# Kernel optimization log

Hardware: AMD Instinct MI355X
Metric: run time of the kernel (lower is better)

## Reference

```python
import jax, jax.numpy as jnp
import numpy as np

H = 16
D_MODEL = 1024
BLOCK_SIZE = 64
B, S = 2, 2048
NEG = -65504.0  # value used by the torch module for masking


def setup_inputs() -> dict:
    key = jax.random.key(0)
    ks = jax.random.split(key, 12)
    scale = 1.0 / np.sqrt(D_MODEL)
    inp = {
        "query": jax.random.normal(ks[0], (B, S, D_MODEL), jnp.float32),
        "key": jax.random.normal(ks[1], (B, S, D_MODEL), jnp.float32),
        "value": jax.random.normal(ks[2], (B, S, D_MODEL), jnp.float32),
        "Wq": jax.random.normal(ks[3], (D_MODEL, D_MODEL), jnp.float32) * scale,
        "bq": jnp.zeros((D_MODEL,), jnp.float32),
        "Wk": jax.random.normal(ks[4], (D_MODEL, D_MODEL), jnp.float32) * scale,
        "bk": jnp.zeros((D_MODEL,), jnp.float32),
        "Wv": jax.random.normal(ks[5], (D_MODEL, D_MODEL), jnp.float32) * scale,
        "bv": jnp.zeros((D_MODEL,), jnp.float32),
        "Wo": jax.random.normal(ks[6], (D_MODEL, D_MODEL), jnp.float32) * scale,
        "bo": jnp.zeros((D_MODEL,), jnp.float32),
    }
    return inp


def reference(query, key, value, Wq, bq, Wk, bk, Wv, bv, Wo, bo):
    b, s, d = query.shape
    dk = d // H

    def proj(x, W, bias):
        # [b,s,d] -> [b,h,s,dk]
        return (x @ W + bias).reshape(b, s, H, dk).transpose(0, 2, 1, 3)

    q = proj(query, Wq, bq)
    k = proj(key, Wk, bk)
    v = proj(value, Wv, bv)

    # dense QK^T / sqrt(d_k), exactly as the torch module (then block mask added)
    scores = jnp.einsum("bhqd,bhkd->bhqk", q, k) / jnp.sqrt(jnp.float32(dk))

    bid = jnp.arange(s) // BLOCK_SIZE
    attn_mask = jnp.where(bid[:, None] == bid[None, :], 0.0, NEG).astype(scores.dtype)
    scores = scores + attn_mask  # broadcast over [b,h]

    attn = jax.nn.softmax(scores, axis=-1)
    x = jnp.einsum("bhqk,bhkd->bhqd", attn, v)
    x = x.transpose(0, 2, 1, 3).reshape(b, s, d)
    return x @ Wo + bo
```

## Files before the change

### kernel.cpp

```cpp
#include <hip/hip_runtime.h>
#include <hip/hip_bf16.h>

typedef __attribute__((ext_vector_type(4))) float f32x4;
typedef __attribute__((ext_vector_type(8))) short s16x8;

#define MFMA16(a, b, c) __builtin_amdgcn_mfma_f32_16x16x32_bf16(a, b, c, 0, 0, 0)

__device__ __forceinline__ void gld_lds16(const void* g, void* l) {
  __builtin_amdgcn_global_load_lds(
      (const __attribute__((address_space(1))) unsigned int*)g,
      (__attribute__((address_space(3))) unsigned int*)l, 16, 0, 0);
}

__device__ __forceinline__ unsigned short f2bf(float f) {
  union { __hip_bfloat16 b; unsigned short u; } cv;
  cv.b = __float2bfloat16(f);
  return cv.u;
}
__device__ __forceinline__ float bf2f(unsigned short u) {
  union { unsigned short u; __hip_bfloat16 b; } cv;
  cv.u = u;
  return __bfloat162float(cv.b);
}

__global__ void transw(const float* W0, unsigned short* H0,
                       const float* W1, unsigned short* H1,
                       const float* W2, unsigned short* H2,
                       const float* W3, unsigned short* H3) {
  __shared__ float tile[64 * 65];
  const float* W; unsigned short* H;
  switch (blockIdx.y) {
    case 0: W = W0; H = H0; break;
    case 1: W = W1; H = H1; break;
    case 2: W = W2; H = H2; break;
    default: W = W3; H = H3; break;
  }
  const int t = threadIdx.x;
  const int tk0 = (blockIdx.x & 15) * 64;
  const int tn0 = (blockIdx.x >> 4) * 64;
  for (int i = 0; i < 16; ++i) {
    int idx = i * 256 + t;
    int r = idx >> 6, c = idx & 63;
    tile[r * 65 + c] = W[(size_t)(tk0 + r) * 1024 + tn0 + c];
  }
  __syncthreads();
  for (int i = 0; i < 16; ++i) {
    int idx = i * 256 + t;
    int r = idx >> 6, c = idx & 63;
    H[(size_t)(tn0 + r) * 1024 + tk0 + c] = f2bf(tile[c * 65 + r]);
  }
}

__global__ void convert_x3(const float* A0, unsigned short* H0,
                           const float* A1, unsigned short* H1,
                           const float* A2, unsigned short* H2) {
  const float* src; unsigned short* h;
  switch (blockIdx.y) {
    case 0: src = A0; h = H0; break;
    case 1: src = A1; h = H1; break;
    default: src = A2; h = H2; break;
  }
  int i = blockIdx.x * 256 + threadIdx.x;
  float4 v = ((const float4*)src)[i];
  ((ushort4*)h)[i] = make_ushort4(f2bf(v.x), f2bf(v.y), f2bf(v.z), f2bf(v.w));
}

struct QkvArgs {
  const unsigned short* A[3];
  const unsigned short* B[3];
  const float* bias[3];
  unsigned short* out[3];
};

__global__ __launch_bounds__(512, 2)
void gemm_qkv(QkvArgs args) {
  const int K = 1024;
  __shared__ __align__(16) unsigned short lds[4][2][8192];
  const int tid = threadIdx.x;
  const int lane = tid & 63, w = tid >> 6;

  const int nwg = 192;
  const int orig = blockIdx.x;
  const int swz = (orig & 7) * (nwg >> 3) + (orig >> 3);
  const int g = swz >> 6;
  const int tl = swz & 63;
  const int m0 = (tl >> 2) * 256, n0 = (tl & 3) * 256;

  const unsigned short* A = args.A[g];
  const unsigned short* B = args.B[g];
  const float* bias = args.bias[g];
  unsigned short* out = args.out[g];

  const int wm = (w >> 2) * 128, wn = (w & 3) * 64;
  const int fr = lane & 15, gh = lane >> 4;

  size_t aoff[2], boff[2]; int dst[2];
  #pragma unroll
  for (int i = 0; i < 2; ++i) {
    const int G = i * 512 + tid;
    const int rp = G >> 3, spr = G & 7;
    const int s = spr ^ (rp & 7);
    const int srow = 2 * rp + (s >> 2), ko = (s & 3) * 8;
    aoff[i] = (size_t)(m0 + srow) * K + ko;
    boff[i] = (size_t)(n0 + srow) * K + ko;
    dst[i] = G * 8;
  }

  auto stageA = [&](int buf, int kt) {
    gld_lds16(A + aoff[0] + kt, &lds[buf][0][dst[0]]);
    gld_lds16(A + aoff[1] + kt, &lds[buf][0][dst[1]]);
  };
  auto stageB = [&](int buf, int kt) {
    gld_lds16(B + boff[0] + kt, &lds[buf][1][dst[0]]);
    gld_lds16(B + boff[1] + kt, &lds[buf][1][dst[1]]);
  };

  f32x4 acc[8][4] = {};
  const int laneoff = (fr >> 1) * 64 + ((((fr & 1) << 2) | gh) ^ (fr >> 1)) * 8;

  stageA(0, 0);  stageB(0, 0);
  stageA(1, 32); stageB(1, 32);
  stageA(2, 64); stageB(2, 64);
  asm volatile("s_waitcnt vmcnt(8)" ::: "memory");
  __builtin_amdgcn_s_barrier();
  __builtin_amdgcn_sched_barrier(0);

  #pragma unroll 1
  for (int t = 0; t < 32; ++t) {
    const int buf = t & 3;
    const unsigned short* La = &lds[buf][0][wm * 32 + laneoff];
    const unsigned short* Lb = &lds[buf][1][wn * 32 + laneoff];
    s16x8 a[8], b[4];

    #pragma unroll
    for (int nt = 0; nt < 4; ++nt) b[nt] = *(const s16x8*)&Lb[nt * 512];
    #pragma unroll
    for (int mt = 0; mt < 4; ++mt) a[mt] = *(const s16x8*)&La[mt * 512];
    if (t <= 28) stageA((t + 3) & 3, (t + 3) * 32);
    __builtin_amdgcn_s_barrier();
    asm volatile("s_waitcnt lgkmcnt(0)" ::: "memory");
    __builtin_amdgcn_sched_barrier(0);
    __builtin_amdgcn_s_setprio(1);
    #pragma unroll
    for (int mt = 0; mt < 4; ++mt)
      #pragma unroll
      for (int nt = 0; nt < 4; ++nt)
        acc[mt][nt] = MFMA16(a[mt], b[nt], acc[mt][nt]);
    __builtin_amdgcn_s_setprio(0);
    __builtin_amdgcn_s_barrier();
    __builtin_amdgcn_sched_barrier(0);

    #pragma unroll
    for (int mt = 4; mt < 8; ++mt) a[mt] = *(const s16x8*)&La[mt * 512];
    if (t <= 28) stageB((t + 3) & 3, (t + 3) * 32);
    __builtin_amdgcn_s_barrier();
    asm volatile("s_waitcnt lgkmcnt(0)" ::: "memory");
    __builtin_amdgcn_sched_barrier(0);
    __builtin_amdgcn_s_setprio(1);
    #pragma unroll
    for (int mt = 4; mt < 8; ++mt)
      #pragma unroll
      for (int nt = 0; nt < 4; ++nt)
        acc[mt][nt] = MFMA16(a[mt], b[nt], acc[mt][nt]);
    __builtin_amdgcn_s_setprio(0);
    if (t < 29)       { asm volatile("s_waitcnt vmcnt(8)" ::: "memory"); }
    else if (t == 29) { asm volatile("s_waitcnt vmcnt(4)" ::: "memory"); }
    else if (t == 30) { asm volatile("s_waitcnt vmcnt(0)" ::: "memory"); }
    __builtin_amdgcn_s_barrier();
    __builtin_amdgcn_sched_barrier(0);
  }

  float bv[4];
  #pragma unroll
  for (int nt = 0; nt < 4; ++nt) bv[nt] = bias[n0 + wn + nt * 16 + fr];
  if (g == 2) {
    #pragma unroll
    for (int mt = 0; mt < 8; ++mt) {
      const int gm = m0 + wm + mt * 16 + (gh << 2);
      const int b2 = gm >> 11, s = gm & 2047;
      #pragma unroll
      for (int nt = 0; nt < 4; ++nt) {
        const int gn = n0 + wn + nt * 16 + fr;
        const int h = gn >> 6, d = gn & 63;
        f32x4 r = acc[mt][nt];
        ushort4 w4 = make_ushort4(f2bf(r[0] + bv[nt]), f2bf(r[1] + bv[nt]),
                                  f2bf(r[2] + bv[nt]), f2bf(r[3] + bv[nt]));
        *(ushort4*)&out[((size_t)((b2 * 16 + h) * 64 + d)) * 2048 + s] = w4;
      }
    }
  } else {
    #pragma unroll
    for (int mt = 0; mt < 8; ++mt) {
      const int gm = m0 + wm + mt * 16 + (gh << 2);
      #pragma unroll
      for (int nt = 0; nt < 4; ++nt) {
        const int gn = n0 + wn + nt * 16 + fr;
        f32x4 r = acc[mt][nt];
        #pragma unroll
        for (int j = 0; j < 4; ++j) {
          const int row = gm + j;
          size_t off = (((size_t)((row >> 11) * 16 + (gn >> 6))) * 2048 + (row & 2047)) * 64 + (gn & 63);
          out[off] = f2bf(r[j] + bv[nt]);
        }
      }
    }
  }
}

__global__ __launch_bounds__(256, 3)
void gemm_oproj(const unsigned short* __restrict__ A, const unsigned short* __restrict__ B,
                const float* __restrict__ bias, float* __restrict__ out) {
  const int K = 1024, N = 1024;
  __shared__ __align__(16) unsigned short lds[3][2][4096];
  const int tid = threadIdx.x;
  const int lane = tid & 63, wid = tid >> 6;

  const int nwg = 256;
  const int orig = blockIdx.x;
  const int swz = (orig & 7) * (nwg >> 3) + (orig >> 3);
  const int m0 = (swz >> 3) * 128, n0 = (swz & 7) * 128;

  const int wm = (wid >> 1) * 64, wn = (wid & 1) * 64;
  const int fr = lane & 15, gh = lane >> 4;

  size_t aoff[2], boff[2]; int dst[2];
  #pragma unroll
  for (int i = 0; i < 2; ++i) {
    const int G = i * 256 + tid;
    const int rp = G >> 3, spr = G & 7;
    const int s = spr ^ (rp & 7);
    const int srow = 2 * rp + (s >> 2), ko = (s & 3) * 8;
    aoff[i] = (size_t)(m0 + srow) * K + ko;
    boff[i] = (size_t)(n0 + srow) * K + ko;
    dst[i] = G * 8;
  }

  auto stage = [&](int buf, int kt) {
    #pragma unroll
    for (int i = 0; i < 2; ++i) {
      gld_lds16(A + aoff[i] + kt, &lds[buf][0][dst[i]]);
      gld_lds16(B + boff[i] + kt, &lds[buf][1][dst[i]]);
    }
  };

  f32x4 acc[4][4] = {};
  const int laneoff = (fr >> 1) * 64 + ((((fr & 1) << 2) | gh) ^ (fr >> 1)) * 8;

  stage(0, 0); stage(1, 32);
  asm volatile("s_waitcnt vmcnt(4)" ::: "memory");
  __builtin_amdgcn_s_barrier();
  __builtin_amdgcn_sched_barrier(0);

  #pragma unroll 1
  for (int t = 0; t < 32; ++t) {
    const int buf = t % 3;
    const unsigned short* La = &lds[buf][0][wm * 32 + laneoff];
    const unsigned short* Lb = &lds[buf][1][wn * 32 + laneoff];
    s16x8 b[4], a[4];
    #pragma unroll
    for (int nt = 0; nt < 4; ++nt) b[nt] = *(const s16x8*)&Lb[nt * 512];
    #pragma unroll
    for (int mt = 0; mt < 4; ++mt) a[mt] = *(const s16x8*)&La[mt * 512];
    if (t <= 29) stage((t + 2) % 3, (t + 2) * 32);
    __builtin_amdgcn_s_barrier();
    asm volatile("s_waitcnt lgkmcnt(0)" ::: "memory");
    __builtin_amdgcn_sched_barrier(0);
    __builtin_amdgcn_s_setprio(1);
    #pragma unroll
    for (int mt = 0; mt < 4; ++mt)
      #pragma unroll
      for (int nt = 0; nt < 4; ++nt)
        acc[mt][nt] = MFMA16(a[mt], b[nt], acc[mt][nt]);
    __builtin_amdgcn_s_setprio(0);
    if (t < 30)       { asm volatile("s_waitcnt vmcnt(4)" ::: "memory"); }
    else if (t == 30) { asm volatile("s_waitcnt vmcnt(0)" ::: "memory"); }
    __builtin_amdgcn_s_barrier();
    __builtin_amdgcn_sched_barrier(0);
  }

  #pragma unroll
  for (int mt = 0; mt < 4; ++mt) {
    const int gm = m0 + wm + mt * 16 + (gh << 2);
    #pragma unroll
    for (int nt = 0; nt < 4; ++nt) {
      const int gn = n0 + wn + nt * 16 + fr;
      const float bvv = bias[gn];
      f32x4 r = acc[mt][nt];
      #pragma unroll
      for (int j = 0; j < 4; ++j)
        out[(size_t)(gm + j) * N + gn] = r[j] + bvv;
    }
  }
}

__global__ __launch_bounds__(256, 2)
void attn_mfma(const unsigned short* __restrict__ Q, const unsigned short* __restrict__ Kb,
               const unsigned short* __restrict__ Vt, unsigned short* __restrict__ X) {
  __shared__ __align__(16) unsigned short qs[4096];
  __shared__ __align__(16) unsigned short ks2[4096];
  __shared__ __align__(16) unsigned short vs[4096];
  __shared__ __align__(16) unsigned short ps[4096];
  const int tid = threadIdx.x, lane = tid & 63, w = tid >> 6;
  const int hb = blockIdx.x >> 5, qb = blockIdx.x & 31;
  const size_t qkbase = ((size_t)hb * 2048 + qb * 64) * 64;
  const size_t vbase = (size_t)hb * 64 * 2048 + qb * 64;

  #pragma unroll
  for (int i = 0; i < 2; ++i) {
    const int G = i * 256 + tid;
    const int row = G >> 3, slot = G & 7;
    const int sg = slot ^ (row & 7);
    gld_lds16(Q + qkbase + row * 64 + sg * 8, &qs[G * 8]);
    gld_lds16(Kb + qkbase + row * 64 + sg * 8, &ks2[G * 8]);
    gld_lds16(Vt + vbase + (size_t)row * 2048 + sg * 8, &vs[G * 8]);
  }
  asm volatile("s_waitcnt vmcnt(0)" ::: "memory");
  __syncthreads();

  const int fr = lane & 15, gh = lane >> 4;
  const int arow = w * 16 + fr;

  s16x8 aq[2], bk[2][4];
  #pragma unroll
  for (int ks = 0; ks < 2; ++ks) {
    aq[ks] = *(const s16x8*)&qs[arow * 64 + (((ks * 4 + gh) ^ (arow & 7)) << 3)];
    #pragma unroll
    for (int nt = 0; nt < 4; ++nt) {
      const int krow = nt * 16 + fr;
      bk[ks][nt] = *(const s16x8*)&ks2[krow * 64 + (((ks * 4 + gh) ^ (krow & 7)) << 3)];
    }
  }
  f32x4 s[4] = {};
  #pragma unroll
  for (int ks = 0; ks < 2; ++ks)
    #pragma unroll
    for (int nt = 0; nt < 4; ++nt)
      s[nt] = MFMA16(aq[ks], bk[ks][nt], s[nt]);

  #pragma unroll
  for (int j = 0; j < 4; ++j) {
    float t0 = s[0][j] * 0.125f, t1 = s[1][j] * 0.125f;
    float t2 = s[2][j] * 0.125f, t3 = s[3][j] * 0.125f;
    float m = fmaxf(fmaxf(t0, t1), fmaxf(t2, t3));
    m = fmaxf(m, __shfl_xor(m, 1, 64));
    m = fmaxf(m, __shfl_xor(m, 2, 64));
    m = fmaxf(m, __shfl_xor(m, 4, 64));
    m = fmaxf(m, __shfl_xor(m, 8, 64));
    t0 = __expf(t0 - m); t1 = __expf(t1 - m);
    t2 = __expf(t2 - m); t3 = __expf(t3 - m);
    float sum = t0 + t1 + t2 + t3;
    sum += __shfl_xor(sum, 1, 64);
    sum += __shfl_xor(sum, 2, 64);
    sum += __shfl_xor(sum, 4, 64);
    sum += __shfl_xor(sum, 8, 64);
    const float r = 1.0f / sum;
    s[0][j] = t0 * r; s[1][j] = t1 * r; s[2][j] = t2 * r; s[3][j] = t3 * r;
  }

  #pragma unroll
  for (int j = 0; j < 4; ++j) {
    const int q = w * 16 + gh * 4 + j;
    #pragma unroll
    for (int nt = 0; nt < 4; ++nt) {
      const int k = nt * 16 + fr;
      ps[q * 64 + (((k >> 3) ^ (q & 7)) << 3) + (k & 7)] = f2bf(s[nt][j]);
    }
  }

  s16x8 ap[2], bv2[2][4];
  #pragma unroll
  for (int ks = 0; ks < 2; ++ks) {
    ap[ks] = *(const s16x8*)&ps[arow * 64 + (((ks * 4 + gh) ^ (arow & 7)) << 3)];
    #pragma unroll
    for (int nt = 0; nt < 4; ++nt) {
      const int drow = nt * 16 + fr;
      bv2[ks][nt] = *(const s16x8*)&vs[drow * 64 + (((ks * 4 + gh) ^ (drow & 7)) << 3)];
    }
  }
  f32x4 x[4] = {};
  #pragma unroll
  for (int ks = 0; ks < 2; ++ks)
    #pragma unroll
    for (int nt = 0; nt < 4; ++nt)
      x[nt] = MFMA16(ap[ks], bv2[ks][nt], x[nt]);

  const int b = hb >> 4, h = hb & 15;
  #pragma unroll
  for (int nt = 0; nt < 4; ++nt)
    #pragma unroll
    for (int j = 0; j < 4; ++j) {
      const int sgl = qb * 64 + w * 16 + gh * 4 + j;
      X[((size_t)(b * 2048 + sgl)) * 1024 + h * 64 + nt * 16 + fr] = f2bf(x[nt][j]);
    }
}

extern "C" void kernel_launch(void* const* d_in, const int* in_sizes, int n_in,
                              void* d_out, int out_size, void* d_ws, size_t ws_size,
                              hipStream_t stream) {
  const float* query = (const float*)d_in[0];
  const float* key   = (const float*)d_in[1];
  const float* value = (const float*)d_in[2];
  const float* Wq = (const float*)d_in[3]; const float* bq = (const float*)d_in[4];
  const float* Wk = (const float*)d_in[5]; const float* bk = (const float*)d_in[6];
  const float* Wv = (const float*)d_in[7]; const float* bv = (const float*)d_in[8];
  const float* Wo = (const float*)d_in[9]; const float* bo = (const float*)d_in[10];
  float* out = (float*)d_out;

  const size_t W_E = 1024 * 1024;
  const size_t X_E = 4096 * 1024;
  unsigned char* p = (unsigned char*)d_ws;
  auto take = [&](size_t bytes) { void* r = (void*)p; p += bytes; return r; };

  unsigned short* wtq = (unsigned short*)take(W_E * 2);
  unsigned short* wtk = (unsigned short*)take(W_E * 2);
  unsigned short* wtv = (unsigned short*)take(W_E * 2);
  unsigned short* wto = (unsigned short*)take(W_E * 2);
  unsigned short* xq = (unsigned short*)take(X_E * 2);
  unsigned short* xk = (unsigned short*)take(X_E * 2);
  unsigned short* xv = (unsigned short*)take(X_E * 2);
  unsigned short* Qb = (unsigned short*)take(X_E * 2);
  unsigned short* Kb = (unsigned short*)take(X_E * 2);
  unsigned short* Vt = (unsigned short*)take(X_E * 2);
  unsigned short* ao = (unsigned short*)take(X_E * 2);
  (void)ws_size; (void)in_sizes; (void)n_in; (void)out_size;

  transw<<<dim3(256, 4), 256, 0, stream>>>(Wq, wtq, Wk, wtk, Wv, wtv, Wo, wto);
  convert_x3<<<dim3(4096, 3), 256, 0, stream>>>(query, xq, key, xk, value, xv);

  QkvArgs qkv = {};
  qkv.A[0] = xq; qkv.B[0] = wtq; qkv.bias[0] = bq; qkv.out[0] = Qb;
  qkv.A[1] = xk; qkv.B[1] = wtk; qkv.bias[1] = bk; qkv.out[1] = Kb;
  qkv.A[2] = xv; qkv.B[2] = wtv; qkv.bias[2] = bv; qkv.out[2] = Vt;
  gemm_qkv<<<dim3(192), 512, 0, stream>>>(qkv);

  attn_mfma<<<dim3(1024), 256, 0, stream>>>(Qb, Kb, Vt, ao);

  gemm_oproj<<<dim3(256), 256, 0, stream>>>(ao, wto, bo, out);
}
```

Before: 85.48 us.

## Stage QKV epilogue through LDS for vectorized stores and simplify main-loop barriers

The QKV projection GEMM now writes its bias-added bf16 tile into LDS (XOR-swizzled for the transposed V layout) and then issues coalesced 16-byte global stores. This replaces the scattered 2-byte and 8-byte per-element writes. The main loop merges the separate A and B staging into one stage call and removes one mid-iteration barrier and lgkmcnt wait from both GEMMs, which reduces synchronisation. The trade-offs are extra LDS traffic and two __syncthreads in the epilogue, and dropping the barrier could let MFMA issue overlap LDS reads without explicit waits (the compiler must insert them).

```diff
diff --git a/kernel.cpp b/kernel.cpp
--- a/kernel.cpp
+++ b/kernel.cpp
@@ -106,11 +106,9 @@
     dst[i] = G * 8;
   }
 
-  auto stageA = [&](int buf, int kt) {
+  auto stage = [&](int buf, int kt) {
     gld_lds16(A + aoff[0] + kt, &lds[buf][0][dst[0]]);
     gld_lds16(A + aoff[1] + kt, &lds[buf][0][dst[1]]);
-  };
-  auto stageB = [&](int buf, int kt) {
     gld_lds16(B + boff[0] + kt, &lds[buf][1][dst[0]]);
     gld_lds16(B + boff[1] + kt, &lds[buf][1][dst[1]]);
   };
@@ -118,9 +116,7 @@
   f32x4 acc[8][4] = {};
   const int laneoff = (fr >> 1) * 64 + ((((fr & 1) << 2) | gh) ^ (fr >> 1)) * 8;
 
-  stageA(0, 0);  stageB(0, 0);
-  stageA(1, 32); stageB(1, 32);
-  stageA(2, 64); stageB(2, 64);
+  stage(0, 0); stage(1, 32); stage(2, 64);
   asm volatile("s_waitcnt vmcnt(8)" ::: "memory");
   __builtin_amdgcn_s_barrier();
   __builtin_amdgcn_sched_barrier(0);
@@ -131,34 +127,14 @@
     const unsigned short* La = &lds[buf][0][wm * 32 + laneoff];
     const unsigned short* Lb = &lds[buf][1][wn * 32 + laneoff];
     s16x8 a[8], b[4];
-
     #pragma unroll
     for (int nt = 0; nt < 4; ++nt) b[nt] = *(const s16x8*)&Lb[nt * 512];
     #pragma unroll
-    for (int mt = 0; mt < 4; ++mt) a[mt] = *(const s16x8*)&La[mt * 512];
-    if (t <= 28) stageA((t + 3) & 3, (t + 3) * 32);
-    __builtin_amdgcn_s_barrier();
-    asm volatile("s_waitcnt lgkmcnt(0)" ::: "memory");
-    __builtin_amdgcn_sched_barrier(0);
+    for (int mt = 0; mt < 8; ++mt) a[mt] = *(const s16x8*)&La[mt * 512];
+    if (t <= 28) stage((t + 3) & 3, (t + 3) * 32);
     __builtin_amdgcn_s_setprio(1);
     #pragma unroll
-    for (int mt = 0; mt < 4; ++mt)
-      #pragma unroll
-      for (int nt = 0; nt < 4; ++nt)
-        acc[mt][nt] = MFMA16(a[mt], b[nt], acc[mt][nt]);
-    __builtin_amdgcn_s_setprio(0);
-    __builtin_amdgcn_s_barrier();
-    __builtin_amdgcn_sched_barrier(0);
-
-    #pragma unroll
-    for (int mt = 4; mt < 8; ++mt) a[mt] = *(const s16x8*)&La[mt * 512];
-    if (t <= 28) stageB((t + 3) & 3, (t + 3) * 32);
-    __builtin_amdgcn_s_barrier();
-    asm volatile("s_waitcnt lgkmcnt(0)" ::: "memory");
-    __builtin_amdgcn_sched_barrier(0);
-    __builtin_amdgcn_s_setprio(1);
-    #pragma unroll
-    for (int mt = 4; mt < 8; ++mt)
+    for (int mt = 0; mt < 8; ++mt)
       #pragma unroll
       for (int nt = 0; nt < 4; ++nt)
         acc[mt][nt] = MFMA16(a[mt], b[nt], acc[mt][nt]);
@@ -173,36 +149,58 @@
   float bv[4];
   #pragma unroll
   for (int nt = 0; nt < 4; ++nt) bv[nt] = bias[n0 + wn + nt * 16 + fr];
+  unsigned short* eb = &lds[0][0][0];
+  __syncthreads();
   if (g == 2) {
     #pragma unroll
-    for (int mt = 0; mt < 8; ++mt) {
-      const int gm = m0 + wm + mt * 16 + (gh << 2);
-      const int b2 = gm >> 11, s = gm & 2047;
+    for (int mt = 0; mt < 8; ++mt)
       #pragma unroll
       for (int nt = 0; nt < 4; ++nt) {
-        const int gn = n0 + wn + nt * 16 + fr;
-        const int h = gn >> 6, d = gn & 63;
-        f32x4 r = acc[mt][nt];
-        ushort4 w4 = make_ushort4(f2bf(r[0] + bv[nt]), f2bf(r[1] + bv[nt]),
-                                  f2bf(r[2] + bv[nt]), f2bf(r[3] + bv[nt]));
-        *(ushort4*)&out[((size_t)((b2 * 16 + h) * 64 + d)) * 2048 + s] = w4;
-      }
-    }
-  } else {
-    #pragma unroll
-    for (int mt = 0; mt < 8; ++mt) {
-      const int gm = m0 + wm + mt * 16 + (gh << 2);
-      #pragma unroll
-      for (int nt = 0; nt < 4; ++nt) {
-        const int gn = n0 + wn + nt * 16 + fr;
+        const int nl = wn + nt * 16 + fr;
         f32x4 r = acc[mt][nt];
         #pragma unroll
         for (int j = 0; j < 4; ++j) {
-          const int row = gm + j;
-          size_t off = (((size_t)((row >> 11) * 16 + (gn >> 6))) * 2048 + (row & 2047)) * 64 + (gn & 63);
-          out[off] = f2bf(r[j] + bv[nt]);
+          const int sl = wm + mt * 16 + gh * 4 + j;
+          eb[sl * 256 + (nl ^ ((sl >> 3) & 31))] = f2bf(r[j] + bv[nt]);
         }
       }
+  } else {
+    #pragma unroll
+    for (int mt = 0; mt < 8; ++mt)
+      #pragma unroll
+      for (int nt = 0; nt < 4; ++nt) {
+        const int nl = wn + nt * 16 + fr;
+        f32x4 r = acc[mt][nt];
+        #pragma unroll
+        for (int j = 0; j < 4; ++j) {
+          const int sl = wm + mt * 16 + gh * 4 + j;
+          eb[sl * 256 + nl] = f2bf(r[j] + bv[nt]);
+        }
+      }
+  }
+  __syncthreads();
+  const int b2 = m0 >> 11;
+  if (g == 2) {
+    #pragma unroll
+    for (int it = 0; it < 16; ++it) {
+      const int u = it * 512 + tid;
+      const int nl = u >> 5, sc = u & 31;
+      s16x8 v;
+      #pragma unroll
+      for (int r = 0; r < 8; ++r)
+        v[r] = (short)eb[(sc * 8 + r) * 256 + (nl ^ sc)];
+      const int gn = n0 + nl, h = gn >> 6, d = gn & 63;
+      *(s16x8*)&out[((size_t)((b2 * 16 + h) * 64 + d)) * 2048 + (m0 & 2047) + sc * 8] = v;
+    }
+  } else {
+    #pragma unroll
+    for (int it = 0; it < 16; ++it) {
+      const int u = it * 512 + tid;
+      const int sl = u >> 5, n8 = (u & 31) * 8;
+      s16x8 v = *(const s16x8*)&eb[sl * 256 + n8];
+      const int s = m0 + sl;
+      const int gn = n0 + n8, h = gn >> 6, d = gn & 63;
+      *(s16x8*)&out[(((size_t)(b2 * 16 + h)) * 2048 + (s & 2047)) * 64 + d] = v;
     }
   }
 }
@@ -262,9 +260,6 @@
     #pragma unroll
     for (int mt = 0; mt < 4; ++mt) a[mt] = *(const s16x8*)&La[mt * 512];
     if (t <= 29) stage((t + 2) % 3, (t + 2) * 32);
-    __builtin_amdgcn_s_barrier();
-    asm volatile("s_waitcnt lgkmcnt(0)" ::: "memory");
-    __builtin_amdgcn_sched_barrier(0);
     __builtin_amdgcn_s_setprio(1);
     #pragma unroll
     for (int mt = 0; mt < 4; ++mt)
```

New measurement: 79.79 us. -6.7%, faster.
